# Kernel tuning notes

Measured on AMD Instinct MI355X. Metric: run time of the kernel, lower is better.

The kernel has to match this reference:

```python
import jax, jax.numpy as jnp
import numpy as np

EPS = 1e-5
BN_GAMMA = 1.0
BN_BETA = 1e-4  # per torch init: BN weight=1, bias=0.0001


def bn(h):
    # BatchNorm1d in training mode: biased batch variance
    mu = h.mean(axis=0)
    var = h.var(axis=0)
    return (h - mu) * (BN_GAMMA / jnp.sqrt(var + EPS)) + BN_BETA


def gcn_conv(h, W, b, row, col, n, edge_weight=None):
    # PyG-style GCNConv: linear -> add self loops (w=1) -> sym deg norm -> scatter-sum
    h = h @ W
    e = row.shape[0]
    ew = jnp.ones((e,), h.dtype) if edge_weight is None else edge_weight
    loop = jnp.arange(n, dtype=row.dtype)
    r = jnp.concatenate([row, loop])
    c = jnp.concatenate([col, loop])
    w = jnp.concatenate([ew, jnp.ones((n,), h.dtype)])
    deg = jax.ops.segment_sum(w, r, num_segments=n)
    dinv = jnp.where(deg > 0, jax.lax.rsqrt(deg + jnp.where(deg > 0, 0.0, 1.0)), 0.0)
    norm = dinv[r] * w * dinv[c]  # [E+N]
    msg = h[r] * norm[:, None]    # gather + per-edge scale
    out = jax.ops.segment_sum(msg, c, num_segments=n)  # scatter-aggregate
    return out + b


def readout(h, W1, b1, W2, b2):
    h = bn(h) @ W1 + b1
    h = bn(jax.nn.relu(h)) @ W2 + b2
    return jax.nn.log_softmax(h, axis=-1)


def setup_inputs() -> dict:
    key = jax.random.key(0)
    ks = jax.random.split(key, 12)
    N, E, F, H, C = 50000, 800000, 128, 128, 10
    s = 0.05
    return {
        "x": jax.random.normal(ks[0], (N, F), jnp.float32),
        "edge_index": jax.random.randint(ks[1], (2, E), 0, N, jnp.int32),
        "perm": jax.random.permutation(ks[2], N).astype(jnp.int32),
        "W_feat": jax.random.normal(ks[3], (F, H), jnp.float32) * s,
        "b_feat": jnp.zeros((H,), jnp.float32),
        "W_convs": jax.random.normal(ks[4], (3, H, H), jnp.float32) * s,
        "b_convs": jnp.zeros((3, H), jnp.float32),
        "W_ea": jax.random.normal(ks[5], (2 * H, 2), jnp.float32) * s,
        "b_ea": jnp.zeros((2,), jnp.float32),
        "W_na": jax.random.normal(ks[6], (H, 2), jnp.float32) * s,
        "b_na": jnp.zeros((2,), jnp.float32),
        "W_ctx": jax.random.normal(ks[7], (H, H), jnp.float32) * s,
        "b_ctx": jnp.zeros((H,), jnp.float32),
        "W_obj": jax.random.normal(ks[8], (H, H), jnp.float32) * s,
        "b_obj": jnp.zeros((H,), jnp.float32),
        "W_fc1": jax.random.normal(ks[9], (3, H, H), jnp.float32) * s,  # c,o,co
        "b_fc1": jnp.zeros((3, H), jnp.float32),
        "W_fc2": jax.random.normal(ks[10], (3, H, C), jnp.float32) * s,
        "b_fc2": jnp.zeros((3, C), jnp.float32),
    }


def reference(x, edge_index, perm, W_feat, b_feat, W_convs, b_convs, W_ea, b_ea,
              W_na, b_na, W_ctx, b_ctx, W_obj, b_obj, W_fc1, b_fc1, W_fc2, b_fc2):
    n = x.shape[0]
    row, col = edge_index[0], edge_index[1]
    h = bn(x)
    h = jax.nn.relu(h @ W_feat + b_feat)  # conv_feat has gfn=True -> pure linear
    for i in range(3):
        h = jax.nn.relu(gcn_conv(bn(h), W_convs[i], b_convs[i], row, col, n))
    edge_rep = jnp.concatenate([h[row], h[col]], axis=-1)  # [E, 2H]
    edge_att = jax.nn.softmax(edge_rep @ W_ea + b_ea, axis=-1)
    node_att = jax.nn.softmax(h @ W_na + b_na, axis=-1)
    xc = node_att[:, 0:1] * h
    xo = node_att[:, 1:2] * h
    xc = jax.nn.relu(gcn_conv(bn(xc), W_ctx, b_ctx, row, col, n, edge_att[:, 0]))
    xo = jax.nn.relu(gcn_conv(bn(xo), W_obj, b_obj, row, col, n, edge_att[:, 1]))
    xc_logis = readout(xc, W_fc1[0], b_fc1[0], W_fc2[0], b_fc2[0])
    xo_logis = readout(xo, W_fc1[1], b_fc1[1], W_fc2[1], b_fc2[1])
    xco_logis = readout(xc[perm] + xo, W_fc1[2], b_fc1[2], W_fc2[2], b_fc2[2])
    return (xc_logis, xo_logis, xco_logis)
```

## Files before the change

kernel.cpp:

```cpp
#include <hip/hip_runtime.h>
#include <math.h>

#define H 128
#define NCLS 10
#define EPS 1e-5f
#define BN_BETA 1e-4f
#define CS_BLOCKS 256

typedef unsigned short u16;
typedef unsigned int u32;
typedef __attribute__((ext_vector_type(8))) short short8;
typedef __attribute__((ext_vector_type(4))) float floatx4;

__device__ inline float bflo(u32 u) { union { u32 i; float f; } a; a.i = u << 16; return a.f; }
__device__ inline float bfhi(u32 u) { union { u32 i; float f; } a; a.i = u & 0xffff0000u; return a.f; }
__device__ inline u16 f2bf(float f) {
  union { float f; u32 i; } v; v.f = f;
  return (u16)((v.i + 0x7fff + ((v.i >> 16) & 1)) >> 16);
}
__device__ inline u32 pack2(float a, float b) { return (u32)f2bf(a) | ((u32)f2bf(b) << 16); }

__device__ inline void reduce_partials(const float* __restrict__ P, int nb, int stride,
                                       int off0, int f, float* su_out, float* sq_out) {
  float su[8] = {0, 0, 0, 0, 0, 0, 0, 0}, sq[8] = {0, 0, 0, 0, 0, 0, 0, 0};
  int b = 0;
  for (; b + 8 <= nb; b += 8) {
#pragma unroll
    for (int u = 0; u < 8; u++) {
      const float* p = P + (size_t)(b + u) * stride + off0;
      su[u] += p[f];
      sq[u] += p[128 + f];
    }
  }
  for (; b < nb; b++) {
    const float* p = P + (size_t)b * stride + off0;
    su[0] += p[f];
    sq[0] += p[128 + f];
  }
  *su_out = ((su[0] + su[1]) + (su[2] + su[3])) + ((su[4] + su[5]) + (su[6] + su[7]));
  *sq_out = ((sq[0] + sq[1]) + (sq[2] + sq[3])) + ((sq[4] + sq[5]) + (sq[6] + sq[7]));
}

__device__ inline void fold256_body(const float* P, int nb, int stride, int off0,
                                    const float* W, const float* bias, float invN,
                                    int kp, u16* Wt, float* cf) {
  int f = threadIdx.x & 127;
  int half = threadIdx.x >> 7;
  int k = kp * 2 + half;
  float su, sq;
  reduce_partials(P, nb, stride, off0, f, &su, &sq);
  float mu = su * invN;
  float var = sq * invN - mu * mu;
  float s = 1.0f / sqrtf(fmaxf(var, 0.f) + EPS);
  float w = W[(size_t)f * H + k];
  Wt[(size_t)k * H + f] = f2bf(s * w);
  __shared__ float red[2][128];
  red[half][f] = (BN_BETA - mu * s) * w;
  __syncthreads();
  for (int o = 64; o > 0; o >>= 1) {
    if (f < o) red[half][f] += red[half][f + o];
    __syncthreads();
  }
  if (f == 0) cf[k] = red[half][0] + (bias ? bias[k] : 0.f);
}

__device__ inline void hist_body(const int* __restrict__ row, const int* __restrict__ col,
                                 int E, int* cnt_in, int* cnt_out,
                                 int* rank_in, int* rank_out, int blk) {
  int e = blk * 256 + threadIdx.x;
  if (e < E) {
    rank_in[e] = atomicAdd(&cnt_in[col[e]], 1);
    rank_out[e] = atomicAdd(&cnt_out[row[e]], 1);
  }
}

__device__ inline void xstats_body(const float* __restrict__ x, int n4,
                                   float* __restrict__ stp, int blk) {
  int tid = threadIdx.x;
  int lane = tid & 63, wave = tid >> 6;
  float s[4] = {0, 0, 0, 0}, q[4] = {0, 0, 0, 0};
  int step = CS_BLOCKS * 256;
  for (int i = blk * 256 + tid; i < n4; i += step) {
    float4 v = ((const float4*)x)[i];
    s[0] += v.x; q[0] += v.x * v.x; s[1] += v.y; q[1] += v.y * v.y;
    s[2] += v.z; q[2] += v.z * v.z; s[3] += v.w; q[3] += v.w * v.w;
  }
#pragma unroll
  for (int k = 0; k < 4; k++) { s[k] += __shfl_xor(s[k], 32); q[k] += __shfl_xor(q[k], 32); }
  __shared__ float smx[4][256];
  int col = (lane & 31) * 4;
  if (lane < 32) {
#pragma unroll
    for (int k = 0; k < 4; k++) { smx[wave][col + k] = s[k]; smx[wave][128 + col + k] = q[k]; }
  }
  __syncthreads();
  stp[(size_t)blk * 256 + tid] = smx[0][tid] + smx[1][tid] + smx[2][tid] + smx[3][tid];
}

__device__ inline void scanA_body(const int* cnt_in, const int* cnt_out, int N,
                                  int* partial_in, int* partial_out, float* dinv, int blk) {
  int i = blk * 256 + threadIdx.x;
  int vo = (i < N) ? cnt_out[i] : 0;
  if (i < N) dinv[i] = 1.0f / sqrtf((float)vo + 1.0f);
  __shared__ int sdA[256];
  sdA[threadIdx.x] = (i < N) ? cnt_in[i] : 0;
  __syncthreads();
  for (int o = 128; o > 0; o >>= 1) {
    if (threadIdx.x < o) sdA[threadIdx.x] += sdA[threadIdx.x + o];
    __syncthreads();
  }
  if (threadIdx.x == 0) partial_in[blk] = sdA[0];
  __syncthreads();
  sdA[threadIdx.x] = vo;
  __syncthreads();
  for (int o = 128; o > 0; o >>= 1) {
    if (threadIdx.x < o) sdA[threadIdx.x] += sdA[threadIdx.x + o];
    __syncthreads();
  }
  if (threadIdx.x == 0) partial_out[blk] = sdA[0];
}

__device__ inline void scanB1(const int* partial, int nb, int* blockoff) {
  __shared__ int sdB[256];
  int t = threadIdx.x;
  int v = (t < nb) ? partial[t] : 0;
  sdB[t] = v;
  __syncthreads();
  for (int o = 1; o < 256; o <<= 1) {
    int x = (t >= o) ? sdB[t - o] : 0;
    __syncthreads();
    sdB[t] += x;
    __syncthreads();
  }
  blockoff[t] = sdB[t] - v;
  __syncthreads();
}

__device__ inline void scanC1(const int* cnt, int N, const int* blockoff,
                              int* off, int E, int blk) {
  __shared__ int sdC[256];
  int t = threadIdx.x;
  int i = blk * 256 + t;
  int v = (i < N) ? cnt[i] : 0;
  sdC[t] = v;
  __syncthreads();
  for (int o = 1; o < 256; o <<= 1) {
    int x = (t >= o) ? sdC[t - o] : 0;
    __syncthreads();
    sdC[t] += x;
    __syncthreads();
  }
  if (i < N) off[i] = blockoff[blk] + sdC[t] - v;
  if (i == 0) off[N] = E;
  __syncthreads();
}

__device__ inline void place_body(const int* row, const int* col, int E,
                                  const int* rank_in, const int* rank_out,
                                  const int* off_in, const int* off_out,
                                  const float* dinv, int* csr_src, int* slot_in,
                                  int* sout, float* wn, int blk) {
  int e = blk * 256 + threadIdx.x;
  if (e < E) {
    int c = col[e], r = row[e];
    int si = off_in[c] + rank_in[e];
    csr_src[si] = r;
    slot_in[e] = si;
    wn[si] = dinv[r];
    sout[e] = off_out[r] + rank_out[e];
  }
}

__device__ inline void eatt_body(const int* row, const int* col, int E,
                                 const float2* p01, const float2* q01,
                                 const float* b_ea, const int* slot_in,
                                 const int* sout, float* att0s, float* att_r, int blk) {
  int e = blk * 256 + threadIdx.x;
  if (e >= E) return;
  int r = row[e], c = col[e];
  float2 p = p01[r], q = q01[c];
  float l0 = p.x + q.x + b_ea[0];
  float l1 = p.y + q.y + b_ea[1];
  float a0 = 1.0f / (1.0f + expf(l1 - l0));
  att0s[slot_in[e]] = a0;
  att_r[sout[e]] = a0;
}

__device__ inline void degsum_body(const float* att_r, const int* off_out,
                                   float* degc, int N, int blk) {
  int v = blk * 256 + threadIdx.x;
  if (v >= N) return;
  int s0 = off_out[v], s1 = off_out[v + 1];
  float s = 0.f;
  for (int i = s0; i < s1; i++) s += att_r[i];
  degc[v] = s;
}

__device__ inline void xprestats_body(const u16* __restrict__ h,
                                      const float2* __restrict__ na01, int n4,
                                      float* __restrict__ stp, int blk) {
  int tid = threadIdx.x;
  int lane = tid & 63, wave = tid >> 6;
  float sc[4] = {0, 0, 0, 0}, qc[4] = {0, 0, 0, 0};
  float so[4] = {0, 0, 0, 0}, qo[4] = {0, 0, 0, 0};
  int step = CS_BLOCKS * 256;
  for (int i = blk * 256 + tid; i < n4; i += step) {
    int n = i >> 5;
    uint2 u = ((const uint2*)h)[i];
    float v0 = bflo(u.x), v1 = bfhi(u.x), v2 = bflo(u.y), v3 = bfhi(u.y);
    float2 ab = na01[n];
    float a = ab.x, b = ab.y;
    float c0 = v0 * a, c1 = v1 * a, c2 = v2 * a, c3 = v3 * a;
    float o0 = v0 * b, o1 = v1 * b, o2 = v2 * b, o3 = v3 * b;
    sc[0] += c0; qc[0] += c0 * c0; sc[1] += c1; qc[1] += c1 * c1;
    sc[2] += c2; qc[2] += c2 * c2; sc[3] += c3; qc[3] += c3 * c3;
    so[0] += o0; qo[0] += o0 * o0; so[1] += o1; qo[1] += o1 * o1;
    so[2] += o2; qo[2] += o2 * o2; so[3] += o3; qo[3] += o3 * o3;
  }
#pragma unroll
  for (int k = 0; k < 4; k++) {
    sc[k] += __shfl_xor(sc[k], 32); qc[k] += __shfl_xor(qc[k], 32);
    so[k] += __shfl_xor(so[k], 32); qo[k] += __shfl_xor(qo[k], 32);
  }
  __shared__ float smp[4][512];
  int col = (lane & 31) * 4;
  if (lane < 32) {
#pragma unroll
    for (int k = 0; k < 4; k++) {
      smp[wave][col + k] = sc[k];
      smp[wave][128 + col + k] = qc[k];
      smp[wave][256 + col + k] = so[k];
      smp[wave][384 + col + k] = qo[k];
    }
  }
  __syncthreads();
  float r0 = smp[0][tid] + smp[1][tid] + smp[2][tid] + smp[3][tid];
  float r1 = smp[0][256 + tid] + smp[1][256 + tid] + smp[2][256 + tid] + smp[3][256 + tid];
  stp[(size_t)blk * 512 + tid] = r0;
  stp[(size_t)blk * 512 + 256 + tid] = r1;
}

__device__ inline void gemm_core(const u16* A, const float* Afp, const u16* Bt,
                                 const float* cf, const float* b2, const float* sumw,
                                 u16* C, int N, int relu, int blk, float* stp) {
  int tid = threadIdx.x;
  int wave = tid >> 6, lane = tid & 63;
  int l15 = lane & 15, quad = lane >> 4;
  int row0 = (blk * 4 + wave) * 16;
  if (row0 >= N && !stp) return;
  int arow = row0 + l15;
  short8 a[4];
  short8 z8 = {0, 0, 0, 0, 0, 0, 0, 0};
  if (Afp) {
#pragma unroll
    for (int k4 = 0; k4 < 4; k4++) {
      if (arow < N) {
        const float* p = Afp + (size_t)arow * H + k4 * 32 + quad * 8;
        float4 f0 = *(const float4*)p;
        float4 f1 = *(const float4*)(p + 4);
        union { short8 s8; u32 u[4]; } cv;
        cv.u[0] = pack2(f0.x, f0.y); cv.u[1] = pack2(f0.z, f0.w);
        cv.u[2] = pack2(f1.x, f1.y); cv.u[3] = pack2(f1.z, f1.w);
        a[k4] = cv.s8;
      } else a[k4] = z8;
    }
  } else {
#pragma unroll
    for (int k4 = 0; k4 < 4; k4++)
      a[k4] = (arow < N) ? *(const short8*)(A + (size_t)arow * H + k4 * 32 + quad * 8) : z8;
  }
  float srow[4];
  if (sumw) {
#pragma unroll
    for (int r = 0; r < 4; r++) {
      int row = row0 + quad * 4 + r;
      srow[r] = (row < N) ? sumw[row] : 0.f;
    }
  }
  float ps[8], pq[8];
#pragma unroll
  for (int nt = 0; nt < 8; nt++) {
    floatx4 acc = {0.f, 0.f, 0.f, 0.f};
    const u16* bp = Bt + (size_t)(nt * 16 + l15) * H + quad * 8;
#pragma unroll
    for (int k4 = 0; k4 < 4; k4++) {
      short8 b = *(const short8*)(bp + k4 * 32);
      acc = __builtin_amdgcn_mfma_f32_16x16x32_bf16(a[k4], b, acc, 0, 0, 0);
    }
    int col = nt * 16 + l15;
    float base = cf[col];
    float bb = b2 ? b2[col] : 0.f;
    float s_ = 0.f, q_ = 0.f;
#pragma unroll
    for (int r = 0; r < 4; r++) {
      int row = row0 + quad * 4 + r;
      if (row < N) {
        float v = acc[r] + (sumw ? srow[r] * base + bb : base);
        if (relu) v = fmaxf(v, 0.f);
        s_ += v; q_ += v * v;
        C[(size_t)row * H + col] = f2bf(v);
      }
    }
    ps[nt] = s_; pq[nt] = q_;
  }
  if (stp) {
    __shared__ float sred[4][256];
#pragma unroll
    for (int nt = 0; nt < 8; nt++) {
      ps[nt] += __shfl_xor(ps[nt], 16); ps[nt] += __shfl_xor(ps[nt], 32);
      pq[nt] += __shfl_xor(pq[nt], 16); pq[nt] += __shfl_xor(pq[nt], 32);
    }
    if (quad == 0) {
#pragma unroll
      for (int nt = 0; nt < 8; nt++) {
        sred[wave][nt * 16 + l15] = ps[nt];
        sred[wave][128 + nt * 16 + l15] = pq[nt];
      }
    }
    __syncthreads();
    stp[(size_t)blk * 256 + tid] =
        sred[0][tid] + sred[1][tid] + sred[2][tid] + sred[3][tid];
  }
}

__global__ __launch_bounds__(256) void hist_xstats_kernel(
    const int* row, const int* col, int E, int* cnt_in, int* cnt_out,
    int* rank_in, int* rank_out, int gE, const float* x, int n4, float* stpX) {
  if ((int)blockIdx.x < gE)
    hist_body(row, col, E, cnt_in, cnt_out, rank_in, rank_out, blockIdx.x);
  else
    xstats_body(x, n4, stpX, blockIdx.x - gE);
}

__global__ __launch_bounds__(256) void scanA_fold_kernel(
    const int* cnt_in, const int* cnt_out, int N, int* partial_in, int* partial_out,
    float* dinv, int SB, const float* stpX, const float* W_feat, const float* b_feat,
    float invN, u16* WtA, float* cfA) {
  if ((int)blockIdx.x < SB)
    scanA_body(cnt_in, cnt_out, N, partial_in, partial_out, dinv, blockIdx.x);
  else
    fold256_body(stpX, CS_BLOCKS, 256, 0, W_feat, b_feat, invN, blockIdx.x - SB, WtA, cfA);
}

__global__ __launch_bounds__(256) void scanB_gemmx_kernel(
    const int* partial_in, const int* partial_out, int nb, int* blockoff_in,
    int* blockoff_out, const float* x, const u16* WtA, const float* cfA, u16* C,
    int N, float* stpG) {
  if (blockIdx.x == 0) {
    scanB1(partial_in, nb, blockoff_in);
    scanB1(partial_out, nb, blockoff_out);
  } else {
    gemm_core(nullptr, x, WtA, cfA, nullptr, nullptr, C, N, 1, blockIdx.x - 1, stpG);
  }
}

__global__ __launch_bounds__(256) void scanC_fold_kernel(
    const int* cnt_in, const int* cnt_out, int N, const int* blockoff_in,
    const int* blockoff_out, int* off_in, int* off_out, int E, int SB,
    const float* stpG, int nbG, const float* Wc, float invN, u16* WtB, float* cfB) {
  if ((int)blockIdx.x < SB) {
    scanC1(cnt_in, N, blockoff_in, off_in, E, blockIdx.x);
    scanC1(cnt_out, N, blockoff_out, off_out, E, blockIdx.x);
  } else {
    fold256_body(stpG, nbG, 256, 0, Wc, nullptr, invN, blockIdx.x - SB, WtB, cfB);
  }
}

__global__ __launch_bounds__(256) void place_gemm_kernel(
    const int* row, const int* col, int E, const int* rank_in, const int* rank_out,
    const int* off_in, const int* off_out, const float* dinv, int* csr_src,
    int* slot_in, int* sout, float* wn, int gE,
    const u16* A, const u16* WtB, const float* cfB, u16* C, int N) {
  if ((int)blockIdx.x < gE)
    place_body(row, col, E, rank_in, rank_out, off_in, off_out, dinv, csr_src,
               slot_in, sout, wn, blockIdx.x);
  else
    gemm_core(A, nullptr, WtB, cfB, nullptr, nullptr, C, N, 0, blockIdx.x - gE, nullptr);
}

__global__ __launch_bounds__(256) void eatt_xpre_kernel(
    const int* row, const int* col, int E, const float2* p01, const float2* q01,
    const float* b_ea, const int* slot_in, const int* sout, float* att0s,
    float* att_r, int gE, const u16* h, const float2* na01, int n4, float* stpPre) {
  if ((int)blockIdx.x < gE)
    eatt_body(row, col, E, p01, q01, b_ea, slot_in, sout, att0s, att_r, blockIdx.x);
  else
    xprestats_body(h, na01, n4, stpPre, blockIdx.x - gE);
}

__global__ __launch_bounds__(256) void degsum_fold2_kernel(
    const float* att_r, const int* off_out, float* degc, int N, int gN,
    const float* stpPre, const float* W_ctx, const float* W_obj, float invN,
    u16* Wt2, float* cf2) {
  if ((int)blockIdx.x < gN)
    degsum_body(att_r, off_out, degc, N, blockIdx.x);
  else {
    int b = blockIdx.x - gN;
    int j = b >> 6, kp = b & 63;
    fold256_body(stpPre, CS_BLOCKS, 512, j * 256, j ? W_obj : W_ctx, nullptr, invN, kp,
                 Wt2 + (size_t)j * H * H, cf2 + j * H);
  }
}

__global__ __launch_bounds__(256) void permadd_fold31_kernel(
    const u16* xc, const u16* xo, const int* perm, u16* outb, int n4, float* stpCO,
    const float* stpG, int nbG, const float* W_fc1, const float* b_fc1, float invN,
    u16* Wt3, float* cf3) {
  int tid = threadIdx.x;
  if ((int)blockIdx.x >= CS_BLOCKS) {
    int b = blockIdx.x - CS_BLOCKS;
    int j = b >> 6, kp = b & 63;
    fold256_body(stpG + (size_t)j * nbG * 256, nbG, 256, 0, W_fc1 + (size_t)j * H * H,
                 b_fc1 + j * H, invN, kp, Wt3 + (size_t)j * H * H, cf3 + j * H);
    return;
  }
  int blk = blockIdx.x;
  int lane = tid & 63, wave = tid >> 6;
  float s[4] = {0, 0, 0, 0}, q[4] = {0, 0, 0, 0};
  int step = CS_BLOCKS * 256;
  for (int i = blk * 256 + tid; i < n4; i += step) {
    int n = i >> 5, k = i & 31;
    int p = perm[n];
    uint2 a = ((const uint2*)xc)[(size_t)p * 32 + k];
    uint2 b = ((const uint2*)xo)[i];
    float f0 = bflo(a.x) + bflo(b.x), f1 = bfhi(a.x) + bfhi(b.x);
    float f2 = bflo(a.y) + bflo(b.y), f3 = bfhi(a.y) + bfhi(b.y);
    ((uint2*)outb)[i] = make_uint2(pack2(f0, f1), pack2(f2, f3));
    s[0] += f0; q[0] += f0 * f0; s[1] += f1; q[1] += f1 * f1;
    s[2] += f2; q[2] += f2 * f2; s[3] += f3; q[3] += f3 * f3;
  }
#pragma unroll
  for (int k = 0; k < 4; k++) { s[k] += __shfl_xor(s[k], 32); q[k] += __shfl_xor(q[k], 32); }
  __shared__ float smq[4][256];
  int col = (lane & 31) * 4;
  if (lane < 32) {
#pragma unroll
    for (int k = 0; k < 4; k++) { smq[wave][col + k] = s[k]; smq[wave][128 + col + k] = q[k]; }
  }
  __syncthreads();
  stpCO[(size_t)blk * 256 + tid] = smq[0][tid] + smq[1][tid] + smq[2][tid] + smq[3][tid];
}

__global__ __launch_bounds__(256) void fold256_kernel(
    const float* P, int nb, const float* W, const float* bias, float invN,
    u16* Wt, float* cf) {
  fold256_body(P, nb, 256, 0, W, bias, invN, blockIdx.x, Wt, cf);
}

__global__ __launch_bounds__(128) void fold10x3_kernel(
    const float* stpZ, int nb, const float* W_fc2, const float* b_fc2, float invN,
    float* W2f, float* c2f) {
  int j = blockIdx.x / NCLS, k = blockIdx.x % NCLS;
  const float* P = stpZ + (size_t)j * nb * 256;
  int f = threadIdx.x;
  float su, sq;
  reduce_partials(P, nb, 256, 0, f, &su, &sq);
  float mu = su * invN;
  float var = sq * invN - mu * mu;
  float s = 1.0f / sqrtf(fmaxf(var, 0.f) + EPS);
  float w = W_fc2[(size_t)j * H * NCLS + (size_t)f * NCLS + k];
  W2f[(size_t)j * H * NCLS + (size_t)f * NCLS + k] = s * w;
  __shared__ float red1[H];
  red1[f] = (BN_BETA - mu * s) * w;
  __syncthreads();
  for (int o = 64; o > 0; o >>= 1) {
    if (f < o) red1[f] += red1[f + o];
    __syncthreads();
  }
  if (f == 0) c2f[j * 16 + k] = red1[0] + b_fc2[j * NCLS + k];
}

__global__ __launch_bounds__(256) void gemm_kernel(
    const u16* A, const u16* Bt, const float* cf, u16* C, int N, int relu) {
  gemm_core(A, nullptr, Bt, cf, nullptr, nullptr, C, N, relu, blockIdx.x, nullptr);
}

__global__ __launch_bounds__(256) void gemm2sw_kernel(
    u16* B0, u16* B1, const u16* Wt2, const float* cf2,
    const float* b0, const float* b1, const float* sw0, const float* sw1,
    int N, int gG, float* stp) {
  int j = blockIdx.x / gG, blk = blockIdx.x % gG;
  u16* Z = j ? B1 : B0;
  gemm_core(Z, nullptr, Wt2 + (size_t)j * H * H, cf2 + j * H, j ? b1 : b0,
            j ? sw1 : sw0, Z, N, 1, blk, stp + (size_t)j * gG * 256);
}

__global__ __launch_bounds__(256) void gemm3_kernel(
    u16* Z0, u16* Z1, u16* Z2, const u16* Wt3, const float* cf3,
    int N, int gG, float* stp) {
  int j = blockIdx.x / gG, blk = blockIdx.x % gG;
  u16* Z = (j == 0) ? Z0 : (j == 1) ? Z1 : Z2;
  gemm_core(Z, nullptr, Wt3 + (size_t)j * H * H, cf3 + j * H, nullptr, nullptr,
            Z, N, 1, blk, stp + (size_t)j * gG * 256);
}

__global__ __launch_bounds__(256) void colstats_kernel(
    const u16* __restrict__ X, int N, float* __restrict__ stp) {
  int tid = threadIdx.x;
  int li = tid & 15, rg = tid >> 4;
  int wave = tid >> 6, lane = tid & 63;
  const uint4* T = (const uint4*)X;
  float s[8] = {0, 0, 0, 0, 0, 0, 0, 0}, q[8] = {0, 0, 0, 0, 0, 0, 0, 0};
  for (int r = blockIdx.x * 16 + rg; r < N; r += CS_BLOCKS * 16) {
    uint4 u = T[(size_t)r * 16 + li];
    float f[8] = {bflo(u.x), bfhi(u.x), bflo(u.y), bfhi(u.y),
                  bflo(u.z), bfhi(u.z), bflo(u.w), bfhi(u.w)};
#pragma unroll
    for (int j = 0; j < 8; j++) { s[j] += f[j]; q[j] += f[j] * f[j]; }
  }
#pragma unroll
  for (int j = 0; j < 8; j++) {
    s[j] += __shfl_xor(s[j], 16); s[j] += __shfl_xor(s[j], 32);
    q[j] += __shfl_xor(q[j], 16); q[j] += __shfl_xor(q[j], 32);
  }
  __shared__ float smc[4][256];
  if ((lane & 48) == 0) {
#pragma unroll
    for (int j = 0; j < 8; j++) {
      smc[wave][li * 8 + j] = s[j];
      smc[wave][128 + li * 8 + j] = q[j];
    }
  }
  __syncthreads();
  stp[(size_t)blockIdx.x * 256 + tid] = smc[0][tid] + smc[1][tid] + smc[2][tid] + smc[3][tid];
}

#define ACC8(A, U, W)                                             \
  A[0] += (W) * bflo(U.x); A[1] += (W) * bfhi(U.x);               \
  A[2] += (W) * bflo(U.y); A[3] += (W) * bfhi(U.y);               \
  A[4] += (W) * bflo(U.z); A[5] += (W) * bfhi(U.z);               \
  A[6] += (W) * bflo(U.w); A[7] += (W) * bfhi(U.w);

__global__ __launch_bounds__(256) void agg_kernel(
    const u16* __restrict__ t, const int* __restrict__ csr_src,
    const float* __restrict__ wseg, const int* __restrict__ off,
    const float* __restrict__ dinv, const float* __restrict__ bias,
    u16* __restrict__ out, int N) {
  int v = blockIdx.x * 4 + (threadIdx.x >> 6);
  if (v >= N) return;
  int lane = threadIdx.x & 63;
  int g = lane >> 4, li = lane & 15;
  const uint4* T = (const uint4*)t;
  float dv = dinv[v];
  float acc[8] = {0.f, 0.f, 0.f, 0.f, 0.f, 0.f, 0.f, 0.f};
  if (g == 0) {
    uint4 u = T[(size_t)v * 16 + li];
    float w0 = dv * dv;
    ACC8(acc, u, w0)
  }
  int s0 = off[v], s1 = off[v + 1];
  for (int s = s0; s < s1; s += 32) {
    int ix[8]; float wv[8];
#pragma unroll
    for (int u = 0; u < 8; u++) {
      int e = s + g + u * 4;
      bool ok = e < s1;
      int e2 = ok ? e : s0;
      ix[u] = csr_src[e2];
      wv[u] = ok ? wseg[e2] : 0.f;
    }
    uint4 uu[8];
#pragma unroll
    for (int u = 0; u < 8; u++) uu[u] = T[(size_t)ix[u] * 16 + li];
#pragma unroll
    for (int u = 0; u < 8; u++) { float w = wv[u] * dv; ACC8(acc, uu[u], w) }
  }
#pragma unroll
  for (int j = 0; j < 8; j++) {
    acc[j] += __shfl_xor(acc[j], 16);
    acc[j] += __shfl_xor(acc[j], 32);
  }
  if (g == 0) {
    float o[8];
#pragma unroll
    for (int j = 0; j < 8; j++) o[j] = fmaxf(acc[j] + bias[li * 8 + j], 0.f);
    uint4 w4;
    w4.x = pack2(o[0], o[1]); w4.y = pack2(o[2], o[3]);
    w4.z = pack2(o[4], o[5]); w4.w = pack2(o[6], o[7]);
    ((uint4*)out)[(size_t)v * 16 + li] = w4;
  }
}

__global__ __launch_bounds__(256) void aggdual_kernel(
    const u16* __restrict__ h, const int* __restrict__ csr_src,
    const float* __restrict__ att0s, const int* __restrict__ cnt_out,
    const float* __restrict__ degc, const float2* __restrict__ na01,
    const int* __restrict__ off,
    u16* __restrict__ gc, u16* __restrict__ go,
    float* __restrict__ sumw_c, float* __restrict__ sumw_o, int N) {
  int v = blockIdx.x * 4 + (threadIdx.x >> 6);
  if (v >= N) return;
  int lane = threadIdx.x & 63;
  int g = lane >> 4, li = lane & 15;
  const uint4* T = (const uint4*)h;
  float dgc = degc[v];
  float dvc = 1.0f / sqrtf(dgc + 1.0f);
  float dvo = 1.0f / sqrtf((float)cnt_out[v] - dgc + 1.0f);
  float ac[8] = {0.f, 0.f, 0.f, 0.f, 0.f, 0.f, 0.f, 0.f};
  float ao[8] = {0.f, 0.f, 0.f, 0.f, 0.f, 0.f, 0.f, 0.f};
  float swc = 0.f, swo = 0.f;
  if (g == 0) {
    uint4 u = T[(size_t)v * 16 + li];
    float2 na = na01[v];
    float wc = dvc * dvc, wo = dvo * dvo;
    float wch = wc * na.x, woh = wo * na.y;
    ACC8(ac, u, wch)
    ACC8(ao, u, woh)
  }
  int s0 = off[v], s1 = off[v + 1];
  for (int s = s0; s < s1; s += 16) {
    int ix[4]; float a0v[4];
#pragma unroll
    for (int u = 0; u < 4; u++) {
      int e = s + g + u * 4;
      bool ok = e < s1;
      int e2 = ok ? e : s0;
      ix[u] = csr_src[e2];
      a0v[u] = ok ? att0s[e2] : 0.f;
      if (!ok) a0v[u] = -1.f;
    }
    uint4 uu[4];
    float2 nav[4];
    float dS[4], dC[4];
#pragma unroll
    for (int u = 0; u < 4; u++) {
      int sidx = ix[u];
      uu[u] = T[(size_t)sidx * 16 + li];
      nav[u] = na01[sidx];
      dS[u] = (float)cnt_out[sidx];
      dC[u] = degc[sidx];
    }
#pragma unroll
    for (int u = 0; u < 4; u++) {
      float a0 = a0v[u];
      bool ok = a0 >= 0.f;
      float r0 = ok ? a0 / sqrtf(dC[u] + 1.0f) : 0.f;
      float r1 = ok ? (1.0f - a0) / sqrtf(dS[u] - dC[u] + 1.0f) : 0.f;
      float wc = r0 * nav[u].x * dvc; ACC8(ac, uu[u], wc)
      float wo = r1 * nav[u].y * dvo; ACC8(ao, uu[u], wo)
      swc += r0; swo += r1;
    }
  }
#pragma unroll
  for (int j = 0; j < 8; j++) {
    ac[j] += __shfl_xor(ac[j], 16); ac[j] += __shfl_xor(ac[j], 32);
    ao[j] += __shfl_xor(ao[j], 16); ao[j] += __shfl_xor(ao[j], 32);
  }
  swc += __shfl_xor(swc, 16); swc += __shfl_xor(swc, 32);
  swo += __shfl_xor(swo, 16); swo += __shfl_xor(swo, 32);
  if (g == 0) {
    uint4 wc4, wo4;
    wc4.x = pack2(ac[0], ac[1]); wc4.y = pack2(ac[2], ac[3]);
    wc4.z = pack2(ac[4], ac[5]); wc4.w = pack2(ac[6], ac[7]);
    wo4.x = pack2(ao[0], ao[1]); wo4.y = pack2(ao[2], ao[3]);
    wo4.z = pack2(ao[4], ao[5]); wo4.w = pack2(ao[6], ao[7]);
    ((uint4*)gc)[(size_t)v * 16 + li] = wc4;
    ((uint4*)go)[(size_t)v * 16 + li] = wo4;
    if (li == 0) {
      sumw_c[v] = dvc * swc + dvc * dvc;
      sumw_o[v] = dvo * swo + dvo * dvo;
    }
  }
}

__global__ __launch_bounds__(256) void natt_kernel(
    const u16* __restrict__ h, int N,
    const float* __restrict__ W_na, const float* __restrict__ b_na,
    const float* __restrict__ W_ea,
    float2* __restrict__ na01, float2* __restrict__ p01, float2* __restrict__ q01) {
  int n = blockIdx.x * 256 + threadIdx.x;
  if (n >= N) return;
  float sa0 = 0, sa1 = 0, sp0 = 0, sp1 = 0, sq0 = 0, sq1 = 0;
  const uint2* hr = (const uint2*)(h + (size_t)n * H);
  for (int c = 0; c < 32; c++) {
    uint2 u = hr[c];
    float v0 = bflo(u.x), v1 = bfhi(u.x), v2 = bflo(u.y), v3 = bfhi(u.y);
    int k = c * 4;
    sa0 += v0 * W_na[k * 2] + v1 * W_na[k * 2 + 2] + v2 * W_na[k * 2 + 4] + v3 * W_na[k * 2 + 6];
    sa1 += v0 * W_na[k * 2 + 1] + v1 * W_na[k * 2 + 3] + v2 * W_na[k * 2 + 5] + v3 * W_na[k * 2 + 7];
    sp0 += v0 * W_ea[k * 2] + v1 * W_ea[k * 2 + 2] + v2 * W_ea[k * 2 + 4] + v3 * W_ea[k * 2 + 6];
    sp1 += v0 * W_ea[k * 2 + 1] + v1 * W_ea[k * 2 + 3] + v2 * W_ea[k * 2 + 5] + v3 * W_ea[k * 2 + 7];
    sq0 += v0 * W_ea[(H + k) * 2] + v1 * W_ea[(H + k) * 2 + 2] + v2 * W_ea[(H + k) * 2 + 4] + v3 * W_ea[(H + k) * 2 + 6];
    sq1 += v0 * W_ea[(H + k) * 2 + 1] + v1 * W_ea[(H + k) * 2 + 3] + v2 * W_ea[(H + k) * 2 + 5] + v3 * W_ea[(H + k) * 2 + 7];
  }
  sa0 += b_na[0]; sa1 += b_na[1];
  float m = fmaxf(sa0, sa1);
  float e0 = expf(sa0 - m), e1 = expf(sa1 - m);
  float inv = 1.f / (e0 + e1);
  na01[n] = make_float2(e0 * inv, e1 * inv);
  p01[n] = make_float2(sp0, sp1);
  q01[n] = make_float2(sq0, sq1);
}

__global__ __launch_bounds__(256) void fc2x3_kernel(
    const u16* __restrict__ z0, const u16* __restrict__ z1, const u16* __restrict__ z2,
    const float* __restrict__ W2f, const float* __restrict__ c2f,
    float* __restrict__ outp, int N, int gN) {
  int j = blockIdx.x / gN, blk = blockIdx.x % gN;
  int n = blk * 256 + threadIdx.x;
  if (n >= N) return;
  const u16* z = (j == 0) ? z0 : (j == 1) ? z1 : z2;
  const float* W2 = W2f + (size_t)j * H * NCLS;
  const float* c2 = c2f + j * 16;
  float* op = outp + (size_t)j * N * NCLS;
  float acc[NCLS];
#pragma unroll
  for (int c = 0; c < NCLS; c++) acc[c] = c2[c];
  const uint2* zr = (const uint2*)(z + (size_t)n * H);
  for (int c4 = 0; c4 < 32; c4++) {
    uint2 u = zr[c4];
    float v[4] = {bflo(u.x), bfhi(u.x), bflo(u.y), bfhi(u.y)};
    int k = c4 * 4;
#pragma unroll
    for (int jj = 0; jj < 4; jj++)
#pragma unroll
      for (int c = 0; c < NCLS; c++) acc[c] += v[jj] * W2[(k + jj) * NCLS + c];
  }
  float m = acc[0];
#pragma unroll
  for (int c = 1; c < NCLS; c++) m = fmaxf(m, acc[c]);
  float s = 0.f;
#pragma unroll
  for (int c = 0; c < NCLS; c++) s += expf(acc[c] - m);
  float lse = logf(s) + m;
#pragma unroll
  for (int c = 0; c < NCLS; c++) op[(size_t)n * NCLS + c] = acc[c] - lse;
}

extern "C" void kernel_launch(void* const* d_in, const int* in_sizes, int n_in,
                              void* d_out, int out_size, void* d_ws, size_t ws_size,
                              hipStream_t stream) {
  const int N = in_sizes[0] / H;
  const int E = in_sizes[1] / 2;
  const float* x = (const float*)d_in[0];
  const int* ei = (const int*)d_in[1];
  const int* row = ei;
  const int* col = ei + E;
  const int* perm = (const int*)d_in[2];
  const float* W_feat = (const float*)d_in[3];
  const float* b_feat = (const float*)d_in[4];
  const float* W_convs = (const float*)d_in[5];
  const float* b_convs = (const float*)d_in[6];
  const float* W_ea = (const float*)d_in[7];
  const float* b_ea = (const float*)d_in[8];
  const float* W_na = (const float*)d_in[9];
  const float* b_na = (const float*)d_in[10];
  const float* W_ctx = (const float*)d_in[11];
  const float* b_ctx = (const float*)d_in[12];
  const float* W_obj = (const float*)d_in[13];
  const float* b_obj = (const float*)d_in[14];
  const float* W_fc1 = (const float*)d_in[15];
  const float* b_fc1 = (const float*)d_in[16];
  const float* W_fc2 = (const float*)d_in[17];
  const float* b_fc2 = (const float*)d_in[18];
  float* out = (float*)d_out;

  const int gG = (N + 63) / 64;
  const int gN = (N + 255) / 256;
  const int gE = (E + 255) / 256;
  const int SB = (N + 255) / 256;
  const int n4 = N * 32;
  const int gAgg = (N + 3) / 4;
  const float invN = 1.0f / (float)N;

  char* base = (char*)d_ws;
  size_t off_b = 0;
  auto alloc = [&](size_t bytes) -> void* {
    void* p = base + off_b;
    off_b = (off_b + bytes + 255) & ~(size_t)255;
    return p;
  };
  size_t NB2 = (size_t)N * H * sizeof(u16);
  u16* bufA = (u16*)alloc(NB2);
  u16* bufB = (u16*)alloc(NB2);
  u16* bufC = (u16*)alloc(NB2);
  u16* bufD = (u16*)alloc(NB2);
  int* cnt_in = (int*)alloc(2 * (size_t)N * 4);
  int* cnt_out = cnt_in + N;
  float* degc = (float*)alloc((size_t)N * 4);
  float* stpX = (float*)alloc((size_t)CS_BLOCKS * 256 * 4);
  float* stpG = (float*)alloc(3 * (size_t)gG * 256 * 4);
  float* stpPre = (float*)alloc((size_t)CS_BLOCKS * 512 * 4);
  float* stpCO = (float*)alloc((size_t)CS_BLOCKS * 256 * 4);
  int* off_in = (int*)alloc(((size_t)N + 1) * 4);
  int* off_out = (int*)alloc(((size_t)N + 1) * 4);
  float* dinv = (float*)alloc((size_t)N * 4);
  float* sumw_c = (float*)alloc((size_t)N * 4);
  float* sumw_o = (float*)alloc((size_t)N * 4);
  float2* na01 = (float2*)alloc((size_t)N * 8);
  float2* p01 = (float2*)alloc((size_t)N * 8);
  float2* q01 = (float2*)alloc((size_t)N * 8);
  int* partial_in = (int*)alloc(256 * 4);
  int* partial_out = (int*)alloc(256 * 4);
  int* blockoff_in = (int*)alloc(256 * 4);
  int* blockoff_out = (int*)alloc(256 * 4);
  u16* WtA = (u16*)alloc((size_t)H * H * 2);
  u16* WtB = (u16*)alloc((size_t)H * H * 2);
  u16* Wt2 = (u16*)alloc(2 * (size_t)H * H * 2);
  u16* Wt3 = (u16*)alloc(3 * (size_t)H * H * 2);
  float* cfA = (float*)alloc(H * 4);
  float* cfB = (float*)alloc(H * 4);
  float* cf2 = (float*)alloc(2 * H * 4);
  float* cf3 = (float*)alloc(3 * H * 4);
  float* W2f = (float*)alloc(3 * (size_t)H * NCLS * 4);
  float* c2f = (float*)alloc(3 * 16 * 4);
  int* rank_in = (int*)alloc((size_t)E * 4);
  int* rank_out = (int*)alloc((size_t)E * 4);
  int* csr_src = (int*)alloc((size_t)E * 4);
  int* slot_in = (int*)alloc((size_t)E * 4);
  int* sout = (int*)alloc((size_t)E * 4);
  float* att0s = (float*)alloc((size_t)E * 4);
  float* att_r = (float*)alloc((size_t)E * 4);
  float* wn = (float*)alloc((size_t)E * 4);

  hipMemsetAsync(cnt_in, 0, 2 * (size_t)N * 4, stream);

  hist_xstats_kernel<<<gE + CS_BLOCKS, 256, 0, stream>>>(
      row, col, E, cnt_in, cnt_out, rank_in, rank_out, gE, x, n4, stpX);
  scanA_fold_kernel<<<SB + 64, 256, 0, stream>>>(
      cnt_in, cnt_out, N, partial_in, partial_out, dinv, SB, stpX, W_feat, b_feat,
      invN, WtA, cfA);
  scanB_gemmx_kernel<<<1 + gG, 256, 0, stream>>>(
      partial_in, partial_out, SB, blockoff_in, blockoff_out, x, WtA, cfA, bufA, N, stpG);
  scanC_fold_kernel<<<SB + 64, 256, 0, stream>>>(
      cnt_in, cnt_out, N, blockoff_in, blockoff_out, off_in, off_out, E, SB,
      stpG, gG, W_convs, invN, WtB, cfB);
  place_gemm_kernel<<<gE + gG, 256, 0, stream>>>(
      row, col, E, rank_in, rank_out, off_in, off_out, dinv, csr_src, slot_in, sout,
      wn, gE, bufA, WtB, cfB, bufB, N);
  agg_kernel<<<gAgg, 256, 0, stream>>>(bufB, csr_src, wn, off_in, dinv, b_convs, bufA, N);

  for (int i = 1; i < 3; ++i) {
    colstats_kernel<<<CS_BLOCKS, 256, 0, stream>>>(bufA, N, stpX);
    fold256_kernel<<<64, 256, 0, stream>>>(stpX, CS_BLOCKS, W_convs + (size_t)i * H * H,
                                           nullptr, invN, WtB, cfB);
    gemm_kernel<<<gG, 256, 0, stream>>>(bufA, WtB, cfB, bufB, N, 0);
    agg_kernel<<<gAgg, 256, 0, stream>>>(bufB, csr_src, wn, off_in, dinv,
                                         b_convs + (size_t)i * H, bufA, N);
  }

  natt_kernel<<<gN, 256, 0, stream>>>(bufA, N, W_na, b_na, W_ea, na01, p01, q01);
  eatt_xpre_kernel<<<gE + CS_BLOCKS, 256, 0, stream>>>(
      row, col, E, p01, q01, b_ea, slot_in, sout, att0s, att_r, gE,
      bufA, na01, n4, stpPre);
  degsum_fold2_kernel<<<gN + 128, 256, 0, stream>>>(
      att_r, off_out, degc, N, gN, stpPre, W_ctx, W_obj, invN, Wt2, cf2);
  aggdual_kernel<<<gAgg, 256, 0, stream>>>(bufA, csr_src, att0s, cnt_out, degc, na01,
                                           off_in, bufC, bufD, sumw_c, sumw_o, N);
  gemm2sw_kernel<<<2 * gG, 256, 0, stream>>>(bufC, bufD, Wt2, cf2, b_ctx, b_obj,
                                             sumw_c, sumw_o, N, gG, stpG);

  permadd_fold31_kernel<<<CS_BLOCKS + 128, 256, 0, stream>>>(
      bufC, bufD, perm, bufA, n4, stpCO, stpG, gG, W_fc1, b_fc1, invN, Wt3, cf3);
  fold256_kernel<<<64, 256, 0, stream>>>(stpCO, CS_BLOCKS, W_fc1 + 2 * (size_t)H * H,
                                         b_fc1 + 2 * H, invN, Wt3 + 2 * (size_t)H * H,
                                         cf3 + 2 * H);
  gemm3_kernel<<<3 * gG, 256, 0, stream>>>(bufC, bufD, bufA, Wt3, cf3, N, gG, stpG);
  fold10x3_kernel<<<3 * NCLS, 128, 0, stream>>>(stpG, gG, W_fc2, b_fc2, invN, W2f, c2f);
  fc2x3_kernel<<<3 * gN, 256, 0, stream>>>(bufC, bufD, bufA, W2f, c2f, out, N, gN);
}
```

Before: 833.2 us.

## Drop outgoing CSR build; use atomic degree sums and padded counters

Measured after the change: 857.9 us. 1.03x slower.

```diff
diff --git a/kernel.cpp b/kernel.cpp
--- a/kernel.cpp
+++ b/kernel.cpp
@@ -6,6 +6,7 @@
 #define EPS 1e-5f
 #define BN_BETA 1e-4f
 #define CS_BLOCKS 256
+#define CPAD 16
 
 typedef unsigned short u16;
 typedef unsigned int u32;
@@ -65,12 +66,12 @@
 }
 
 __device__ inline void hist_body(const int* __restrict__ row, const int* __restrict__ col,
-                                 int E, int* cnt_in, int* cnt_out,
-                                 int* rank_in, int* rank_out, int blk) {
+                                 int E, int* cnt_in_p, int* cnt_out_p,
+                                 int* rank_in, int blk) {
   int e = blk * 256 + threadIdx.x;
   if (e < E) {
-    rank_in[e] = atomicAdd(&cnt_in[col[e]], 1);
-    rank_out[e] = atomicAdd(&cnt_out[row[e]], 1);
+    rank_in[e] = atomicAdd(&cnt_in_p[(size_t)col[e] * CPAD], 1);
+    atomicAdd(&cnt_out_p[(size_t)row[e] * CPAD], 1);
   }
 }
 
@@ -97,27 +98,22 @@
   stp[(size_t)blk * 256 + tid] = smx[0][tid] + smx[1][tid] + smx[2][tid] + smx[3][tid];
 }
 
-__device__ inline void scanA_body(const int* cnt_in, const int* cnt_out, int N,
-                                  int* partial_in, int* partial_out, float* dinv, int blk) {
+__device__ inline void scanA_body(const int* cnt_in_p, const int* cnt_out_p, int N,
+                                  int* partial_in, float* dinv, int* degS, int blk) {
   int i = blk * 256 + threadIdx.x;
-  int vo = (i < N) ? cnt_out[i] : 0;
-  if (i < N) dinv[i] = 1.0f / sqrtf((float)vo + 1.0f);
+  int vo = (i < N) ? cnt_out_p[(size_t)i * CPAD] : 0;
+  if (i < N) {
+    dinv[i] = 1.0f / sqrtf((float)vo + 1.0f);
+    degS[i] = vo;
+  }
   __shared__ int sdA[256];
-  sdA[threadIdx.x] = (i < N) ? cnt_in[i] : 0;
+  sdA[threadIdx.x] = (i < N) ? cnt_in_p[(size_t)i * CPAD] : 0;
   __syncthreads();
   for (int o = 128; o > 0; o >>= 1) {
     if (threadIdx.x < o) sdA[threadIdx.x] += sdA[threadIdx.x + o];
     __syncthreads();
   }
   if (threadIdx.x == 0) partial_in[blk] = sdA[0];
-  __syncthreads();
-  sdA[threadIdx.x] = vo;
-  __syncthreads();
-  for (int o = 128; o > 0; o >>= 1) {
-    if (threadIdx.x < o) sdA[threadIdx.x] += sdA[threadIdx.x + o];
-    __syncthreads();
-  }
-  if (threadIdx.x == 0) partial_out[blk] = sdA[0];
 }
 
 __device__ inline void scanB1(const int* partial, int nb, int* blockoff) {
@@ -136,12 +132,12 @@
   __syncthreads();
 }
 
-__device__ inline void scanC1(const int* cnt, int N, const int* blockoff,
+__device__ inline void scanC1(const int* cnt_p, int N, const int* blockoff,
                               int* off, int E, int blk) {
   __shared__ int sdC[256];
   int t = threadIdx.x;
   int i = blk * 256 + t;
-  int v = (i < N) ? cnt[i] : 0;
+  int v = (i < N) ? cnt_p[(size_t)i * CPAD] : 0;
   sdC[t] = v;
   __syncthreads();
   for (int o = 1; o < 256; o <<= 1) {
@@ -156,10 +152,9 @@
 }
 
 __device__ inline void place_body(const int* row, const int* col, int E,
-                                  const int* rank_in, const int* rank_out,
-                                  const int* off_in, const int* off_out,
+                                  const int* rank_in, const int* off_in,
                                   const float* dinv, int* csr_src, int* slot_in,
-                                  int* sout, float* wn, int blk) {
+                                  float* wn, int blk) {
   int e = blk * 256 + threadIdx.x;
   if (e < E) {
     int c = col[e], r = row[e];
@@ -167,14 +162,13 @@
     csr_src[si] = r;
     slot_in[e] = si;
     wn[si] = dinv[r];
-    sout[e] = off_out[r] + rank_out[e];
   }
 }
 
 __device__ inline void eatt_body(const int* row, const int* col, int E,
                                  const float2* p01, const float2* q01,
                                  const float* b_ea, const int* slot_in,
-                                 const int* sout, float* att0s, float* att_r, int blk) {
+                                 float* att0s, float* degc, int blk) {
   int e = blk * 256 + threadIdx.x;
   if (e >= E) return;
   int r = row[e], c = col[e];
@@ -183,17 +177,7 @@
   float l1 = p.y + q.y + b_ea[1];
   float a0 = 1.0f / (1.0f + expf(l1 - l0));
   att0s[slot_in[e]] = a0;
-  att_r[sout[e]] = a0;
-}
-
-__device__ inline void degsum_body(const float* att_r, const int* off_out,
-                                   float* degc, int N, int blk) {
-  int v = blk * 256 + threadIdx.x;
-  if (v >= N) return;
-  int s0 = off_out[v], s1 = off_out[v + 1];
-  float s = 0.f;
-  for (int i = s0; i < s1; i++) s += att_r[i];
-  degc[v] = s;
+  atomicAdd(&degc[r], a0);
 }
 
 __device__ inline void xprestats_body(const u16* __restrict__ h,
@@ -324,82 +308,73 @@
 }
 
 __global__ __launch_bounds__(256) void hist_xstats_kernel(
-    const int* row, const int* col, int E, int* cnt_in, int* cnt_out,
-    int* rank_in, int* rank_out, int gE, const float* x, int n4, float* stpX) {
+    const int* row, const int* col, int E, int* cnt_in_p, int* cnt_out_p,
+    int* rank_in, int gE, const float* x, int n4, float* stpX) {
   if ((int)blockIdx.x < gE)
-    hist_body(row, col, E, cnt_in, cnt_out, rank_in, rank_out, blockIdx.x);
+    hist_body(row, col, E, cnt_in_p, cnt_out_p, rank_in, blockIdx.x);
   else
     xstats_body(x, n4, stpX, blockIdx.x - gE);
 }
 
 __global__ __launch_bounds__(256) void scanA_fold_kernel(
-    const int* cnt_in, const int* cnt_out, int N, int* partial_in, int* partial_out,
-    float* dinv, int SB, const float* stpX, const float* W_feat, const float* b_feat,
-    float invN, u16* WtA, float* cfA) {
+    const int* cnt_in_p, const int* cnt_out_p, int N, int* partial_in,
+    float* dinv, int* degS, int SB, const float* stpX, const float* W_feat,
+    const float* b_feat, float invN, u16* WtA, float* cfA) {
   if ((int)blockIdx.x < SB)
-    scanA_body(cnt_in, cnt_out, N, partial_in, partial_out, dinv, blockIdx.x);
+    scanA_body(cnt_in_p, cnt_out_p, N, partial_in, dinv, degS, blockIdx.x);
   else
     fold256_body(stpX, CS_BLOCKS, 256, 0, W_feat, b_feat, invN, blockIdx.x - SB, WtA, cfA);
 }
 
 __global__ __launch_bounds__(256) void scanB_gemmx_kernel(
-    const int* partial_in, const int* partial_out, int nb, int* blockoff_in,
-    int* blockoff_out, const float* x, const u16* WtA, const float* cfA, u16* C,
+    const int* partial_in, int nb, int* blockoff_in,
+    const float* x, const u16* WtA, const float* cfA, u16* C,
     int N, float* stpG) {
   if (blockIdx.x == 0) {
     scanB1(partial_in, nb, blockoff_in);
-    scanB1(partial_out, nb, blockoff_out);
   } else {
     gemm_core(nullptr, x, WtA, cfA, nullptr, nullptr, C, N, 1, blockIdx.x - 1, stpG);
   }
 }
 
 __global__ __launch_bounds__(256) void scanC_fold_kernel(
-    const int* cnt_in, const int* cnt_out, int N, const int* blockoff_in,
-    const int* blockoff_out, int* off_in, int* off_out, int E, int SB,
+    const int* cnt_in_p, int N, const int* blockoff_in, int* off_in, int E, int SB,
     const float* stpG, int nbG, const float* Wc, float invN, u16* WtB, float* cfB) {
   if ((int)blockIdx.x < SB) {
-    scanC1(cnt_in, N, blockoff_in, off_in, E, blockIdx.x);
-    scanC1(cnt_out, N, blockoff_out, off_out, E, blockIdx.x);
+    scanC1(cnt_in_p, N, blockoff_in, off_in, E, blockIdx.x);
   } else {
     fold256_body(stpG, nbG, 256, 0, Wc, nullptr, invN, blockIdx.x - SB, WtB, cfB);
   }
 }
 
 __global__ __launch_bounds__(256) void place_gemm_kernel(
-    const int* row, const int* col, int E, const int* rank_in, const int* rank_out,
-    const int* off_in, const int* off_out, const float* dinv, int* csr_src,
-    int* slot_in, int* sout, float* wn, int gE,
+    const int* row, const int* col, int E, const int* rank_in,
+    const int* off_in, const float* dinv, int* csr_src,
+    int* slot_in, float* wn, int gE,
     const u16* A, const u16* WtB, const float* cfB, u16* C, int N) {
   if ((int)blockIdx.x < gE)
-    place_body(row, col, E, rank_in, rank_out, off_in, off_out, dinv, csr_src,
-               slot_in, sout, wn, blockIdx.x);
+    place_body(row, col, E, rank_in, off_in, dinv, csr_src, slot_in, wn, blockIdx.x);
   else
     gemm_core(A, nullptr, WtB, cfB, nullptr, nullptr, C, N, 0, blockIdx.x - gE, nullptr);
 }
 
 __global__ __launch_bounds__(256) void eatt_xpre_kernel(
     const int* row, const int* col, int E, const float2* p01, const float2* q01,
-    const float* b_ea, const int* slot_in, const int* sout, float* att0s,
-    float* att_r, int gE, const u16* h, const float2* na01, int n4, float* stpPre) {
+    const float* b_ea, const int* slot_in, float* att0s, float* degc,
+    int gE, const u16* h, const float2* na01, int n4, float* stpPre) {
   if ((int)blockIdx.x < gE)
-    eatt_body(row, col, E, p01, q01, b_ea, slot_in, sout, att0s, att_r, blockIdx.x);
+    eatt_body(row, col, E, p01, q01, b_ea, slot_in, att0s, degc, blockIdx.x);
   else
     xprestats_body(h, na01, n4, stpPre, blockIdx.x - gE);
 }
 
-__global__ __launch_bounds__(256) void degsum_fold2_kernel(
-    const float* att_r, const int* off_out, float* degc, int N, int gN,
+__global__ __launch_bounds__(256) void fold2_kernel(
     const float* stpPre, const float* W_ctx, const float* W_obj, float invN,
     u16* Wt2, float* cf2) {
-  if ((int)blockIdx.x < gN)
-    degsum_body(att_r, off_out, degc, N, blockIdx.x);
-  else {
-    int b = blockIdx.x - gN;
-    int j = b >> 6, kp = b & 63;
-    fold256_body(stpPre, CS_BLOCKS, 512, j * 256, j ? W_obj : W_ctx, nullptr, invN, kp,
-                 Wt2 + (size_t)j * H * H, cf2 + j * H);
-  }
+  int b = blockIdx.x;
+  int j = b >> 6, kp = b & 63;
+  fold256_body(stpPre, CS_BLOCKS, 512, j * 256, j ? W_obj : W_ctx, nullptr, invN, kp,
+               Wt2 + (size_t)j * H * H, cf2 + j * H);
 }
 
 __global__ __launch_bounds__(256) void permadd_fold31_kernel(
@@ -583,7 +558,7 @@
 
 __global__ __launch_bounds__(256) void aggdual_kernel(
     const u16* __restrict__ h, const int* __restrict__ csr_src,
-    const float* __restrict__ att0s, const int* __restrict__ cnt_out,
+    const float* __restrict__ att0s, const int* __restrict__ degS,
     const float* __restrict__ degc, const float2* __restrict__ na01,
     const int* __restrict__ off,
     u16* __restrict__ gc, u16* __restrict__ go,
@@ -595,7 +570,7 @@
   const uint4* T = (const uint4*)h;
   float dgc = degc[v];
   float dvc = 1.0f / sqrtf(dgc + 1.0f);
-  float dvo = 1.0f / sqrtf((float)cnt_out[v] - dgc + 1.0f);
+  float dvo = 1.0f / sqrtf((float)degS[v] - dgc + 1.0f);
   float ac[8] = {0.f, 0.f, 0.f, 0.f, 0.f, 0.f, 0.f, 0.f};
   float ao[8] = {0.f, 0.f, 0.f, 0.f, 0.f, 0.f, 0.f, 0.f};
   float swc = 0.f, swo = 0.f;
@@ -627,7 +602,7 @@
       int sidx = ix[u];
       uu[u] = T[(size_t)sidx * 16 + li];
       nav[u] = na01[sidx];
-      dS[u] = (float)cnt_out[sidx];
+      dS[u] = (float)degS[sidx];
       dC[u] = degc[sidx];
     }
 #pragma unroll
@@ -775,15 +750,16 @@
   u16* bufB = (u16*)alloc(NB2);
   u16* bufC = (u16*)alloc(NB2);
   u16* bufD = (u16*)alloc(NB2);
-  int* cnt_in = (int*)alloc(2 * (size_t)N * 4);
-  int* cnt_out = cnt_in + N;
-  float* degc = (float*)alloc((size_t)N * 4);
+  int* zeroblk = (int*)alloc(((size_t)2 * CPAD * N + N) * 4);
+  int* cnt_in_p = zeroblk;
+  int* cnt_out_p = zeroblk + (size_t)CPAD * N;
+  float* degc = (float*)(zeroblk + (size_t)2 * CPAD * N);
+  int* degS = (int*)alloc((size_t)N * 4);
   float* stpX = (float*)alloc((size_t)CS_BLOCKS * 256 * 4);
   float* stpG = (float*)alloc(3 * (size_t)gG * 256 * 4);
   float* stpPre = (float*)alloc((size_t)CS_BLOCKS * 512 * 4);
   float* stpCO = (float*)alloc((size_t)CS_BLOCKS * 256 * 4);
   int* off_in = (int*)alloc(((size_t)N + 1) * 4);
-  int* off_out = (int*)alloc(((size_t)N + 1) * 4);
   float* dinv = (float*)alloc((size_t)N * 4);
   float* sumw_c = (float*)alloc((size_t)N * 4);
   float* sumw_o = (float*)alloc((size_t)N * 4);
@@ -791,9 +767,7 @@
   float2* p01 = (float2*)alloc((size_t)N * 8);
   float2* q01 = (float2*)alloc((size_t)N * 8);
   int* partial_in = (int*)alloc(256 * 4);
-  int* partial_out = (int*)alloc(256 * 4);
   int* blockoff_in = (int*)alloc(256 * 4);
-  int* blockoff_out = (int*)alloc(256 * 4);
   u16* WtA = (u16*)alloc((size_t)H * H * 2);
   u16* WtB = (u16*)alloc((size_t)H * H * 2);
   u16* Wt2 = (u16*)alloc(2 * (size_t)H * H * 2);
@@ -805,29 +779,25 @@
   float* W2f = (float*)alloc(3 * (size_t)H * NCLS * 4);
   float* c2f = (float*)alloc(3 * 16 * 4);
   int* rank_in = (int*)alloc((size_t)E * 4);
-  int* rank_out = (int*)alloc((size_t)E * 4);
   int* csr_src = (int*)alloc((size_t)E * 4);
   int* slot_in = (int*)alloc((size_t)E * 4);
-  int* sout = (int*)alloc((size_t)E * 4);
   float* att0s = (float*)alloc((size_t)E * 4);
-  float* att_r = (float*)alloc((size_t)E * 4);
   float* wn = (float*)alloc((size_t)E * 4);
 
-  hipMemsetAsync(cnt_in, 0, 2 * (size_t)N * 4, stream);
+  hipMemsetAsync(zeroblk, 0, ((size_t)2 * CPAD * N + N) * 4, stream);
 
   hist_xstats_kernel<<<gE + CS_BLOCKS, 256, 0, stream>>>(
-      row, col, E, cnt_in, cnt_out, rank_in, rank_out, gE, x, n4, stpX);
+      row, col, E, cnt_in_p, cnt_out_p, rank_in, gE, x, n4, stpX);
   scanA_fold_kernel<<<SB + 64, 256, 0, stream>>>(
-      cnt_in, cnt_out, N, partial_in, partial_out, dinv, SB, stpX, W_feat, b_feat,
+      cnt_in_p, cnt_out_p, N, partial_in, dinv, degS, SB, stpX, W_feat, b_feat,
       invN, WtA, cfA);
   scanB_gemmx_kernel<<<1 + gG, 256, 0, stream>>>(
-      partial_in, partial_out, SB, blockoff_in, blockoff_out, x, WtA, cfA, bufA, N, stpG);
+      partial_in, SB, blockoff_in, x, WtA, cfA, bufA, N, stpG);
   scanC_fold_kernel<<<SB + 64, 256, 0, stream>>>(
-      cnt_in, cnt_out, N, blockoff_in, blockoff_out, off_in, off_out, E, SB,
-      stpG, gG, W_convs, invN, WtB, cfB);
+      cnt_in_p, N, blockoff_in, off_in, E, SB, stpG, gG, W_convs, invN, WtB, cfB);
   place_gemm_kernel<<<gE + gG, 256, 0, stream>>>(
-      row, col, E, rank_in, rank_out, off_in, off_out, dinv, csr_src, slot_in, sout,
-      wn, gE, bufA, WtB, cfB, bufB, N);
+      row, col, E, rank_in, off_in, dinv, csr_src, slot_in, wn, gE,
+      bufA, WtB, cfB, bufB, N);
   agg_kernel<<<gAgg, 256, 0, stream>>>(bufB, csr_src, wn, off_in, dinv, b_convs, bufA, N);
 
   for (int i = 1; i < 3; ++i) {
@@ -841,11 +811,10 @@
 
   natt_kernel<<<gN, 256, 0, stream>>>(bufA, N, W_na, b_na, W_ea, na01, p01, q01);
   eatt_xpre_kernel<<<gE + CS_BLOCKS, 256, 0, stream>>>(
-      row, col, E, p01, q01, b_ea, slot_in, sout, att0s, att_r, gE,
+      row, col, E, p01, q01, b_ea, slot_in, att0s, degc, gE,
       bufA, na01, n4, stpPre);
-  degsum_fold2_kernel<<<gN + 128, 256, 0, stream>>>(
-      att_r, off_out, degc, N, gN, stpPre, W_ctx, W_obj, invN, Wt2, cf2);
-  aggdual_kernel<<<gAgg, 256, 0, stream>>>(bufA, csr_src, att0s, cnt_out, degc, na01,
+  fold2_kernel<<<128, 256, 0, stream>>>(stpPre, W_ctx, W_obj, invN, Wt2, cf2);
+  aggdual_kernel<<<gAgg, 256, 0, stream>>>(bufA, csr_src, att0s, degS, degc, na01,
                                            off_in, bufC, bufD, sumw_c, sumw_o, N);
   gemm2sw_kernel<<<2 * gG, 256, 0, stream>>>(bufC, bufD, Wt2, cf2, b_ctx, b_obj,
                                              sumw_c, sumw_o, N, gG, stpG);
```
